# Kernel tuning notes

Hardware: AMD Instinct MI355X
Metric: run time of the kernel (lower is better)

## Reference

```python
import jax, jax.numpy as jnp
import numpy as np

SIREN_W0 = 1.0
OUTPUT_BIAS = 0.0
EPS = 1e-12  # F.normalize eps


def setup_inputs() -> dict:
    key = jax.random.key(0)
    ks = jax.random.split(key, 12)
    inp = {}
    inp["coord"] = jax.random.uniform(ks[0], (4, 1, 256, 256, 3), dtype=jnp.float32)
    inp["pixel_latent"] = jax.random.normal(ks[1], (4, 64, 64, 32), dtype=jnp.float32)
    # base params linear_wb{i}: (fan_in, fan_out), last row is bias
    wshapes = [(36, 128), (129, 128), (129, 128), (129, 128), (129, 2)]
    for i, s in enumerate(wshapes):
        inp[f"w{i}"] = jax.random.normal(ks[2 + i], s, dtype=jnp.float32) * 0.1
    # modulations: (B, fan_in-1, fan_out)
    mshapes = [(4, 35, 128), (4, 128, 128), (4, 128, 128), (4, 128, 128), (4, 128, 2)]
    for i, s in enumerate(mshapes):
        inp[f"m{i}"] = jax.random.normal(ks[7 + i], s, dtype=jnp.float32)
    return inp


def _hyponet_forward(coord, pixel_latent, weights, mods):
    B = coord.shape[0]
    coord_shape = coord.shape[1:-1]  # (T=1, H, W)
    H, W = coord_shape[1], coord_shape[2]
    C = pixel_latent.shape[-1]
    # bilinear interp (half-pixel centers == torch align_corners=False)
    lat = jax.image.resize(pixel_latent, (B, H, W, C), method="bilinear")
    hidden = jnp.concatenate(
        [lat.reshape(B, -1, C), coord.reshape(B, -1, coord.shape[-1])], axis=-1
    )  # [B, N, 35]
    n_layer = len(weights)
    for i, (w, m) in enumerate(zip(weights, mods)):
        ones = jnp.ones((*hidden.shape[:-1], 1), dtype=hidden.dtype)
        hidden = jnp.concatenate([hidden, ones], axis=-1)  # append bias input
        pw = w[None, :-1, :] * m  # modulated weight [B, fan_in-1, fan_out]
        # F.normalize over dim=1
        norm = jnp.sqrt(jnp.sum(pw * pw, axis=1, keepdims=True))
        pw = pw / jnp.maximum(norm, EPS)
        bias_row = jnp.broadcast_to(w[None, -1:, :], (B, 1, w.shape[1]))
        param = jnp.concatenate([pw, bias_row], axis=1)  # [B, fan_in, fan_out]
        hidden = jnp.einsum("bnf,bfo->bno", hidden, param)
        if i < n_layer - 1:
            hidden = jnp.sin(SIREN_W0 * hidden)
    out = hidden + OUTPUT_BIAS
    return out.reshape(B, *coord_shape, -1)


def reference(coord, pixel_latent, w0, w1, w2, w3, w4, m0, m1, m2, m3, m4):
    return _hyponet_forward(
        coord, pixel_latent, [w0, w1, w2, w3, w4], [m0, m1, m2, m3, m4]
    )
```

## Files before the change

kernel.cpp:

```cpp
#include <hip/hip_runtime.h>
#include <math.h>

#define OFF0 0
#define OFF1 18432
#define OFF2 83968
#define OFF3 149504
#define OFF4 215040
#define OFFB 216064

__global__ void prep_params(
    const float* __restrict__ w0, const float* __restrict__ w1,
    const float* __restrict__ w2, const float* __restrict__ w3,
    const float* __restrict__ w4,
    const float* __restrict__ m0, const float* __restrict__ m1,
    const float* __restrict__ m2, const float* __restrict__ m3,
    const float* __restrict__ m4,
    float* __restrict__ ws)
{
    int idx = blockIdx.x * blockDim.x + threadIdx.x;
    if (idx >= 2056) return;
    int layer, b, o;
    if (idx < 2048) { layer = idx >> 9; b = (idx >> 7) & 3; o = idx & 127; }
    else { layer = 4; int r = idx - 2048; b = r >> 1; o = r & 1; }

    const float* w; const float* m; int Fm, O, Fp; int off;
    switch (layer) {
      case 0:  w = w0; m = m0; Fm = 35;  O = 128; Fp = 36;  off = OFF0; break;
      case 1:  w = w1; m = m1; Fm = 128; O = 128; Fp = 128; off = OFF1; break;
      case 2:  w = w2; m = m2; Fm = 128; O = 128; Fp = 128; off = OFF2; break;
      case 3:  w = w3; m = m3; Fm = 128; O = 128; Fp = 128; off = OFF3; break;
      default: w = w4; m = m4; Fm = 128; O = 2;   Fp = 128; off = OFF4; break;
    }

    float ss = 0.f;
    for (int f = 0; f < Fm; ++f) {
        float v = w[f * O + o] * m[(b * Fm + f) * O + o];
        ss += v * v;
    }
    float r = 1.0f / fmaxf(sqrtf(ss), 1e-12f);

    float* pT = ws + off + (b * O + o) * Fp;
    for (int f = 0; f < Fm; ++f) {
        float v = w[f * O + o] * m[(b * Fm + f) * O + o];
        pT[f] = v * r;
    }
    if (layer == 0) pT[35] = 0.f;
    ws[OFFB + layer * 512 + b * 128 + o] = w[Fm * O + o];
}

template<int F>
__device__ __forceinline__ void accum2p(const float* __restrict__ r0,
                                        const float* __restrict__ r1, int s,
                                        const float* __restrict__ pb,
                                        const float* __restrict__ bs,
                                        float* a0, float* a1)
{
    #pragma unroll
    for (int j = 0; j < 8; ++j) { a0[j] = bs[j]; a1[j] = bs[j]; }
    #pragma unroll 2
    for (int k = 0; k < (F + 3) / 4; ++k) {
        const int off = ((k ^ s) << 2);
        float4 h0 = *(const float4*)(r0 + off);
        float4 h1 = *(const float4*)(r1 + off);
        #pragma unroll
        for (int j = 0; j < 8; ++j) {
            const float* pr = pb + j * F + k * 4;
            a0[j] = fmaf(h0.x, pr[0], a0[j]);  a1[j] = fmaf(h1.x, pr[0], a1[j]);
            a0[j] = fmaf(h0.y, pr[1], a0[j]);  a1[j] = fmaf(h1.y, pr[1], a1[j]);
            a0[j] = fmaf(h0.z, pr[2], a0[j]);  a1[j] = fmaf(h1.z, pr[2], a1[j]);
            a0[j] = fmaf(h0.w, pr[3], a0[j]);  a1[j] = fmaf(h1.w, pr[3], a1[j]);
        }
    }
}

__device__ __forceinline__ float4 interp_pt(const float* __restrict__ lat,
                                            int b, int pg, int c0)
{
    const int y = pg >> 8, x = pg & 255;
    const float sy = (y + 0.5f) * 0.25f - 0.5f;
    const float sx = (x + 0.5f) * 0.25f - 0.5f;
    const float fy = floorf(sy), fx = floorf(sx);
    const float ty = sy - fy, tx = sx - fx;
    int y0 = (int)fy, x0 = (int)fx;
    const int y1 = min(y0 + 1, 63); y0 = max(y0, 0);
    const int x1 = min(x0 + 1, 63); x0 = max(x0, 0);
    const float* base = lat + ((size_t)b << 17) + c0;
    const float4 v00 = *(const float4*)(base + (y0 * 64 + x0) * 32);
    const float4 v01 = *(const float4*)(base + (y0 * 64 + x1) * 32);
    const float4 v10 = *(const float4*)(base + (y1 * 64 + x0) * 32);
    const float4 v11 = *(const float4*)(base + (y1 * 64 + x1) * 32);
    const float w00 = (1.f - ty) * (1.f - tx), w01 = (1.f - ty) * tx;
    const float w10 = ty * (1.f - tx),         w11 = ty * tx;
    float4 r;
    r.x = w00 * v00.x + w01 * v01.x + w10 * v10.x + w11 * v11.x;
    r.y = w00 * v00.y + w01 * v01.y + w10 * v10.y + w11 * v11.y;
    r.z = w00 * v00.z + w01 * v01.z + w10 * v10.z + w11 * v11.z;
    r.w = w00 * v00.w + w01 * v01.w + w10 * v10.w + w11 * v11.w;
    return r;
}

__global__ __launch_bounds__(512, 4)
void hyponet_main(const float* __restrict__ coord,
                  const float* __restrict__ lat,
                  const float* __restrict__ ws,
                  float* __restrict__ out)
{
    __shared__ float hsf[128 * 128];
    const int tid  = threadIdx.x;
    const int lane = tid & 63;
    const int wv   = tid >> 6;
    const int b    = blockIdx.x >> 9;
    const int tile = blockIdx.x & 511;
    const int pg0  = tile * 128 + lane;
    const int pg1  = pg0 + 64;
    const int s    = lane & 31;
    float* r0 = hsf + lane * 128;
    float* r1 = r0 + 64 * 128;

    {
        const int c0 = wv * 4;
        *(float4*)(r0 + (((wv) ^ s) << 2)) = interp_pt(lat, b, pg0, c0);
        *(float4*)(r1 + (((wv) ^ s) << 2)) = interp_pt(lat, b, pg1, c0);
        if (wv == 0) {
            const float* cp0 = coord + ((size_t)b * 65536 + pg0) * 3;
            const float* cp1 = coord + ((size_t)b * 65536 + pg1) * 3;
            *(float4*)(r0 + ((8 ^ s) << 2)) = make_float4(cp0[0], cp0[1], cp0[2], 0.f);
            *(float4*)(r1 + ((8 ^ s) << 2)) = make_float4(cp1[0], cp1[1], cp1[2], 0.f);
        }
    }
    __syncthreads();

    const int ob0 = __builtin_amdgcn_readfirstlane(wv * 16);
    const int ob1 = __builtin_amdgcn_readfirstlane(wv * 16 + 8);
    float a0[16], a1[16];

    {
        accum2p<36>(r0, r1, s, ws + OFF0 + (b * 128 + ob0) * 36,
                    ws + OFFB + b * 128 + ob0, a0, a1);
        accum2p<36>(r0, r1, s, ws + OFF0 + (b * 128 + ob1) * 36,
                    ws + OFFB + b * 128 + ob1, a0 + 8, a1 + 8);
        #pragma unroll
        for (int j = 0; j < 16; ++j) { a0[j] = __sinf(a0[j]); a1[j] = __sinf(a1[j]); }
        __syncthreads();
        #pragma unroll
        for (int jj = 0; jj < 4; ++jj) {
            const int off = (((wv * 4 + jj) ^ s) << 2);
            *(float4*)(r0 + off) = make_float4(a0[jj*4], a0[jj*4+1], a0[jj*4+2], a0[jj*4+3]);
            *(float4*)(r1 + off) = make_float4(a1[jj*4], a1[jj*4+1], a1[jj*4+2], a1[jj*4+3]);
        }
        __syncthreads();
    }

    #pragma unroll 1
    for (int L = 1; L <= 3; ++L) {
        const int off_w = (L == 1) ? OFF1 : (L == 2) ? OFF2 : OFF3;
        accum2p<128>(r0, r1, s, ws + off_w + (b * 128 + ob0) * 128,
                     ws + OFFB + L * 512 + b * 128 + ob0, a0, a1);
        accum2p<128>(r0, r1, s, ws + off_w + (b * 128 + ob1) * 128,
                     ws + OFFB + L * 512 + b * 128 + ob1, a0 + 8, a1 + 8);
        #pragma unroll
        for (int j = 0; j < 16; ++j) { a0[j] = __sinf(a0[j]); a1[j] = __sinf(a1[j]); }
        __syncthreads();
        #pragma unroll
        for (int jj = 0; jj < 4; ++jj) {
            const int off = (((wv * 4 + jj) ^ s) << 2);
            *(float4*)(r0 + off) = make_float4(a0[jj*4], a0[jj*4+1], a0[jj*4+2], a0[jj*4+3]);
            *(float4*)(r1 + off) = make_float4(a1[jj*4], a1[jj*4+1], a1[jj*4+2], a1[jj*4+3]);
        }
        __syncthreads();
    }

    if (wv < 2) {
        const float* hl = (wv == 0) ? r0 : r1;
        const float* pb = ws + OFF4 + b * 2 * 128;
        const float* bs = ws + OFFB + 4 * 512 + b * 128;
        float q0 = bs[0], q1 = bs[1];
        #pragma unroll 2
        for (int k = 0; k < 32; ++k) {
            float4 h = *(const float4*)(hl + ((k ^ s) << 2));
            const float* w0r = pb + k * 4;
            const float* w1r = pb + 128 + k * 4;
            q0 = fmaf(h.x, w0r[0], q0); q1 = fmaf(h.x, w1r[0], q1);
            q0 = fmaf(h.y, w0r[1], q0); q1 = fmaf(h.y, w1r[1], q1);
            q0 = fmaf(h.z, w0r[2], q0); q1 = fmaf(h.z, w1r[2], q1);
            q0 = fmaf(h.w, w0r[3], q0); q1 = fmaf(h.w, w1r[3], q1);
        }
        const int pt = tile * 128 + wv * 64 + lane;
        *(float2*)&out[((size_t)b * 65536 + pt) * 2] = make_float2(q0, q1);
    }
}

extern "C" void kernel_launch(void* const* d_in, const int* in_sizes, int n_in,
                              void* d_out, int out_size, void* d_ws, size_t ws_size,
                              hipStream_t stream)
{
    const float* coord = (const float*)d_in[0];
    const float* lat   = (const float*)d_in[1];
    float* ws = (float*)d_ws;

    prep_params<<<9, 256, 0, stream>>>(
        (const float*)d_in[2], (const float*)d_in[3], (const float*)d_in[4],
        (const float*)d_in[5], (const float*)d_in[6],
        (const float*)d_in[7], (const float*)d_in[8], (const float*)d_in[9],
        (const float*)d_in[10], (const float*)d_in[11], ws);

    hyponet_main<<<2048, 512, 0, stream>>>(coord, lat, ws, (float*)d_out);
}
```

Before: 414.6 us.

## Process four points per thread with a 256-point tile per block

Each block now handles 256 points instead of 128. Each thread accumulates four points per output neuron, sharing every scalar weight load across four rows of hidden activations. The activation tile moves to 128 KB of dynamic LDS, and launch bounds drop to 2. This halves the number of weight fetches per FMA. The cost is a doubled accumulator register footprint and likely only one block per CU, which lowers occupancy and the ability to hide latency.

New measurement: 465.1 us. 1.12x slower.

```diff
diff --git a/kernel.cpp b/kernel.cpp
--- a/kernel.cpp
+++ b/kernel.cpp
@@ -49,26 +49,31 @@
 }
 
 template<int F>
-__device__ __forceinline__ void accum2p(const float* __restrict__ r0,
-                                        const float* __restrict__ r1, int s,
+__device__ __forceinline__ void accum4p(const float* __restrict__ rb, int s,
                                         const float* __restrict__ pb,
                                         const float* __restrict__ bs,
-                                        float* a0, float* a1)
+                                        float* a0, float* a1, float* a2, float* a3)
 {
     #pragma unroll
-    for (int j = 0; j < 8; ++j) { a0[j] = bs[j]; a1[j] = bs[j]; }
+    for (int j = 0; j < 8; ++j) { a0[j] = bs[j]; a1[j] = bs[j]; a2[j] = bs[j]; a3[j] = bs[j]; }
     #pragma unroll 2
     for (int k = 0; k < (F + 3) / 4; ++k) {
         const int off = ((k ^ s) << 2);
-        float4 h0 = *(const float4*)(r0 + off);
-        float4 h1 = *(const float4*)(r1 + off);
+        float4 h0 = *(const float4*)(rb + off);
+        float4 h1 = *(const float4*)(rb + 8192 + off);
+        float4 h2 = *(const float4*)(rb + 16384 + off);
+        float4 h3 = *(const float4*)(rb + 24576 + off);
         #pragma unroll
         for (int j = 0; j < 8; ++j) {
             const float* pr = pb + j * F + k * 4;
             a0[j] = fmaf(h0.x, pr[0], a0[j]);  a1[j] = fmaf(h1.x, pr[0], a1[j]);
+            a2[j] = fmaf(h2.x, pr[0], a2[j]);  a3[j] = fmaf(h3.x, pr[0], a3[j]);
             a0[j] = fmaf(h0.y, pr[1], a0[j]);  a1[j] = fmaf(h1.y, pr[1], a1[j]);
+            a2[j] = fmaf(h2.y, pr[1], a2[j]);  a3[j] = fmaf(h3.y, pr[1], a3[j]);
             a0[j] = fmaf(h0.z, pr[2], a0[j]);  a1[j] = fmaf(h1.z, pr[2], a1[j]);
+            a2[j] = fmaf(h2.z, pr[2], a2[j]);  a3[j] = fmaf(h3.z, pr[2], a3[j]);
             a0[j] = fmaf(h0.w, pr[3], a0[j]);  a1[j] = fmaf(h1.w, pr[3], a1[j]);
+            a2[j] = fmaf(h2.w, pr[3], a2[j]);  a3[j] = fmaf(h3.w, pr[3], a3[j]);
         }
     }
 }
@@ -99,79 +104,76 @@
     return r;
 }
 
-__global__ __launch_bounds__(512, 4)
+__global__ __launch_bounds__(512, 2)
 void hyponet_main(const float* __restrict__ coord,
                   const float* __restrict__ lat,
                   const float* __restrict__ ws,
                   float* __restrict__ out)
 {
-    __shared__ float hsf[128 * 128];
+    extern __shared__ float hsf[];
     const int tid  = threadIdx.x;
     const int lane = tid & 63;
     const int wv   = tid >> 6;
-    const int b    = blockIdx.x >> 9;
-    const int tile = blockIdx.x & 511;
-    const int pg0  = tile * 128 + lane;
-    const int pg1  = pg0 + 64;
+    const int b    = blockIdx.x >> 8;
+    const int tile = blockIdx.x & 255;
+    const int pgB  = tile * 256;
     const int s    = lane & 31;
-    float* r0 = hsf + lane * 128;
-    float* r1 = r0 + 64 * 128;
+    float* rb = hsf + lane * 128;
 
     {
         const int c0 = wv * 4;
-        *(float4*)(r0 + (((wv) ^ s) << 2)) = interp_pt(lat, b, pg0, c0);
-        *(float4*)(r1 + (((wv) ^ s) << 2)) = interp_pt(lat, b, pg1, c0);
+        #pragma unroll
+        for (int j = 0; j < 4; ++j)
+            *(float4*)(rb + j * 8192 + ((wv ^ s) << 2)) =
+                interp_pt(lat, b, pgB + j * 64 + lane, c0);
         if (wv == 0) {
-            const float* cp0 = coord + ((size_t)b * 65536 + pg0) * 3;
-            const float* cp1 = coord + ((size_t)b * 65536 + pg1) * 3;
-            *(float4*)(r0 + ((8 ^ s) << 2)) = make_float4(cp0[0], cp0[1], cp0[2], 0.f);
-            *(float4*)(r1 + ((8 ^ s) << 2)) = make_float4(cp1[0], cp1[1], cp1[2], 0.f);
+            #pragma unroll
+            for (int j = 0; j < 4; ++j) {
+                const float* cp = coord + ((size_t)b * 65536 + pgB + j * 64 + lane) * 3;
+                *(float4*)(rb + j * 8192 + ((8 ^ s) << 2)) =
+                    make_float4(cp[0], cp[1], cp[2], 0.f);
+            }
         }
     }
     __syncthreads();
 
     const int ob0 = __builtin_amdgcn_readfirstlane(wv * 16);
     const int ob1 = __builtin_amdgcn_readfirstlane(wv * 16 + 8);
-    float a0[16], a1[16];
-
-    {
-        accum2p<36>(r0, r1, s, ws + OFF0 + (b * 128 + ob0) * 36,
-                    ws + OFFB + b * 128 + ob0, a0, a1);
-        accum2p<36>(r0, r1, s, ws + OFF0 + (b * 128 + ob1) * 36,
-                    ws + OFFB + b * 128 + ob1, a0 + 8, a1 + 8);
-        #pragma unroll
-        for (int j = 0; j < 16; ++j) { a0[j] = __sinf(a0[j]); a1[j] = __sinf(a1[j]); }
+    float a0[16], a1[16], a2[16], a3[16];
+
+    #pragma unroll 1
+    for (int L = 0; L <= 3; ++L) {
+        if (L == 0) {
+            accum4p<36>(rb, s, ws + OFF0 + (b * 128 + ob0) * 36,
+                        ws + OFFB + b * 128 + ob0, a0, a1, a2, a3);
+            accum4p<36>(rb, s, ws + OFF0 + (b * 128 + ob1) * 36,
+                        ws + OFFB + b * 128 + ob1, a0 + 8, a1 + 8, a2 + 8, a3 + 8);
+        } else {
+            const int off_w = (L == 1) ? OFF1 : (L == 2) ? OFF2 : OFF3;
+            accum4p<128>(rb, s, ws + off_w + (b * 128 + ob0) * 128,
+                         ws + OFFB + L * 512 + b * 128 + ob0, a0, a1, a2, a3);
+            accum4p<128>(rb, s, ws + off_w + (b * 128 + ob1) * 128,
+                         ws + OFFB + L * 512 + b * 128 + ob1, a0 + 8, a1 + 8, a2 + 8, a3 + 8);
+        }
+        #pragma unroll
+        for (int j = 0; j < 16; ++j) {
+            a0[j] = __sinf(a0[j]); a1[j] = __sinf(a1[j]);
+            a2[j] = __sinf(a2[j]); a3[j] = __sinf(a3[j]);
+        }
         __syncthreads();
         #pragma unroll
         for (int jj = 0; jj < 4; ++jj) {
             const int off = (((wv * 4 + jj) ^ s) << 2);
-            *(float4*)(r0 + off) = make_float4(a0[jj*4], a0[jj*4+1], a0[jj*4+2], a0[jj*4+3]);
-            *(float4*)(r1 + off) = make_float4(a1[jj*4], a1[jj*4+1], a1[jj*4+2], a1[jj*4+3]);
+            *(float4*)(rb + off)         = make_float4(a0[jj*4], a0[jj*4+1], a0[jj*4+2], a0[jj*4+3]);
+            *(float4*)(rb + 8192 + off)  = make_float4(a1[jj*4], a1[jj*4+1], a1[jj*4+2], a1[jj*4+3]);
+            *(float4*)(rb + 16384 + off) = make_float4(a2[jj*4], a2[jj*4+1], a2[jj*4+2], a2[jj*4+3]);
+            *(float4*)(rb + 24576 + off) = make_float4(a3[jj*4], a3[jj*4+1], a3[jj*4+2], a3[jj*4+3]);
         }
         __syncthreads();
     }
 
-    #pragma unroll 1
-    for (int L = 1; L <= 3; ++L) {
-        const int off_w = (L == 1) ? OFF1 : (L == 2) ? OFF2 : OFF3;
-        accum2p<128>(r0, r1, s, ws + off_w + (b * 128 + ob0) * 128,
-                     ws + OFFB + L * 512 + b * 128 + ob0, a0, a1);
-        accum2p<128>(r0, r1, s, ws + off_w + (b * 128 + ob1) * 128,
-                     ws + OFFB + L * 512 + b * 128 + ob1, a0 + 8, a1 + 8);
-        #pragma unroll
-        for (int j = 0; j < 16; ++j) { a0[j] = __sinf(a0[j]); a1[j] = __sinf(a1[j]); }
-        __syncthreads();
-        #pragma unroll
-        for (int jj = 0; jj < 4; ++jj) {
-            const int off = (((wv * 4 + jj) ^ s) << 2);
-            *(float4*)(r0 + off) = make_float4(a0[jj*4], a0[jj*4+1], a0[jj*4+2], a0[jj*4+3]);
-            *(float4*)(r1 + off) = make_float4(a1[jj*4], a1[jj*4+1], a1[jj*4+2], a1[jj*4+3]);
-        }
-        __syncthreads();
-    }
-
-    if (wv < 2) {
-        const float* hl = (wv == 0) ? r0 : r1;
+    if (wv < 4) {
+        const float* hl = rb + wv * 8192;
         const float* pb = ws + OFF4 + b * 2 * 128;
         const float* bs = ws + OFFB + 4 * 512 + b * 128;
         float q0 = bs[0], q1 = bs[1];
@@ -185,7 +187,7 @@
             q0 = fmaf(h.z, w0r[2], q0); q1 = fmaf(h.z, w1r[2], q1);
             q0 = fmaf(h.w, w0r[3], q0); q1 = fmaf(h.w, w1r[3], q1);
         }
-        const int pt = tile * 128 + wv * 64 + lane;
+        const int pt = pgB + wv * 64 + lane;
         *(float2*)&out[((size_t)b * 65536 + pt) * 2] = make_float2(q0, q1);
     }
 }
@@ -197,6 +199,9 @@
     const float* coord = (const float*)d_in[0];
     const float* lat   = (const float*)d_in[1];
     float* ws = (float*)d_ws;
+
+    (void)hipFuncSetAttribute((const void*)hyponet_main,
+                              hipFuncAttributeMaxDynamicSharedMemorySize, 131072);
 
     prep_params<<<9, 256, 0, stream>>>(
         (const float*)d_in[2], (const float*)d_in[3], (const float*)d_in[4],
@@ -204,5 +209,5 @@
         (const float*)d_in[7], (const float*)d_in[8], (const float*)d_in[9],
         (const float*)d_in[10], (const float*)d_in[11], ws);
 
-    hyponet_main<<<2048, 512, 0, stream>>>(coord, lat, ws, (float*)d_out);
-}
+    hyponet_main<<<1024, 512, 131072, stream>>>(coord, lat, ws, (float*)d_out);
+}
```
